# Performance work log

Hardware: AMD Instinct MI355X
Metric: run time of the kernel (lower is better)

The kernel has to match this reference:

```python
import jax, jax.numpy as jnp
import numpy as np


def _lstm_dir(xz, Uh, reverse):
    """Run one LSTM direction. xz: [B,T,4U] = x@W + b precomputed. Uh: [U,4U].
    activation='sigmoid' (replaces tanh on candidate and cell output),
    recurrent_activation='sigmoid' (Keras default). Gate order: i, f, g, o."""
    B = xz.shape[0]
    units = Uh.shape[0]
    h0 = jnp.zeros((B, units), xz.dtype)
    c0 = jnp.zeros((B, units), xz.dtype)

    def step(carry, z_t):
        h, c = carry
        z = z_t + h @ Uh                      # [B,4U]
        i, f, g, o = jnp.split(z, 4, axis=-1)
        i = jax.nn.sigmoid(i)
        f = jax.nn.sigmoid(f)
        g = jax.nn.sigmoid(g)                 # activation='sigmoid'
        o = jax.nn.sigmoid(o)
        c = f * c + i * g
        h = o * jax.nn.sigmoid(c)             # output activation also sigmoid
        return (h, c), h

    xz_t = jnp.swapaxes(xz, 0, 1)             # [T,B,4U]
    _, hs = jax.lax.scan(step, (h0, c0), xz_t, reverse=reverse)
    return jnp.swapaxes(hs, 0, 1)             # [B,T,U], time-ordered


def setup_inputs() -> dict:
    key = jax.random.key(0)
    k1, k2, k3 = jax.random.split(key, 3)
    B, T, D = 16, 1024, 1024
    L, U = 5, 512
    x = jax.random.normal(k1, (B, T, D), dtype=jnp.float32)
    # Glorot-ish scaling to keep sigmoids out of deep saturation
    W = jax.random.normal(k2, (L, 2, D, 4 * U), dtype=jnp.float32) * 0.03
    Uh = jax.random.normal(k3, (L, 2, U, 4 * U), dtype=jnp.float32) * 0.03
    b = jnp.zeros((L, 2, 4 * U), dtype=jnp.float32)
    return {"x": x, "W": W, "Uh": Uh, "b": b}


def reference(x, W, Uh, b):
    y = x
    n_layers = W.shape[0]
    for l in range(n_layers):
        outs = []
        for d, rev in ((0, False), (1, True)):
            # input projection for all timesteps at once (one big GEMM)
            xz = jnp.einsum('bti,io->bto', y, W[l, d]) + b[l, d]
            outs.append(_lstm_dir(xz, Uh[l, d], rev))
        y = jnp.concatenate(outs, axis=-1)    # Bidirectional merge_mode='concat'
    return y
```

## Files before the change

### kernel.cpp

```cpp
#include <hip/hip_runtime.h>
#include <hip/hip_bf16.h>
#include <stdint.h>


typedef __attribute__((ext_vector_type(8))) short short8;
typedef __attribute__((ext_vector_type(4))) float f32x4;

union U128 { uint4 u; short8 s; };
static __device__ __forceinline__ short8 as_short8(uint4 v) { U128 x; x.u = v; return x.s; }

static __device__ __forceinline__ float sigf(float x) { return 1.0f / (1.0f + __expf(-x)); }

static __device__ __forceinline__ uint32_t f2bfbits(float f) {
  union { float f; uint32_t u; } x; x.f = f;
  return (x.u + 0x7fffu + ((x.u >> 16) & 1u)) >> 16;
}
static __device__ __forceinline__ float bflo(uint32_t v) {
  union { uint32_t u; float f; } x; x.u = v << 16; return x.f;
}
static __device__ __forceinline__ float bfhi(uint32_t v) {
  union { uint32_t u; float f; } x; x.u = v & 0xffff0000u; return x.f;
}

__global__ __launch_bounds__(256) void f32_to_bf16_k(const float* __restrict__ in,
                                                     __hip_bfloat16* __restrict__ out,
                                                     int n4) {
  int i = blockIdx.x * 256 + threadIdx.x;
  if (i < n4) {
    float4 v = ((const float4*)in)[i];
    uint32_t lo = f2bfbits(v.x) | (f2bfbits(v.y) << 16);
    uint32_t hi = f2bfbits(v.z) | (f2bfbits(v.w) << 16);
    ((uint2*)out)[i] = make_uint2(lo, hi);
  }
}

__global__ __launch_bounds__(256) void transpose_bf16_k(const float* __restrict__ in,
                                                        __hip_bfloat16* __restrict__ outp,
                                                        int R) {
  __shared__ float tile[64][65];
  int d = blockIdx.z;
  int k0 = blockIdx.x * 64;
  int c0 = blockIdx.y * 64;
  const float* inb = in + (size_t)d * R * 2048;
  __hip_bfloat16* ob = outp + (size_t)d * 2048 * R;
  int col = threadIdx.x & 63, rr = threadIdx.x >> 6;
#pragma unroll
  for (int i = 0; i < 16; ++i) {
    int r = rr + i * 4;
    tile[r][col] = inb[(size_t)(k0 + r) * 2048 + c0 + col];
  }
  __syncthreads();
#pragma unroll
  for (int i = 0; i < 16; ++i) {
    int r = rr + i * 4;
    ob[(size_t)(c0 + r) * R + k0 + col] = __float2bfloat16(tile[col][r]);
  }
}

__global__ __launch_bounds__(256) void gemm_xz_k(const __hip_bfloat16* __restrict__ y,
                                                 const __hip_bfloat16* __restrict__ Wt,
                                                 const float* __restrict__ bias,
                                                 __hip_bfloat16* __restrict__ xz) {
  __shared__ uint4 Asl[8 * 2 * 64];
  __shared__ uint4 Bsl[8 * 2 * 64];
  int m0 = blockIdx.x * 128;
  int dir = blockIdx.y >> 4;
  int n0 = (blockIdx.y & 15) * 128;
  int tid = threadIdx.x, lane = tid & 63, wv = tid >> 6;
  int wm = wv & 1, wn = wv >> 1;
  const __hip_bfloat16* Wd = Wt + (size_t)dir * 2048 * 1024;
  f32x4 acc[4][4] = {};
  for (int kb = 0; kb < 1024; kb += 64) {
    __syncthreads();
#pragma unroll
    for (int i = 0; i < 4; ++i) {
      int slot = i * 256 + tid;
      int ln = slot & 63, kc = (slot >> 6) & 1, mt = slot >> 7;
      int row = mt * 16 + (ln & 15);
      int kk = kc * 32 + (ln >> 4) * 8;
      Asl[slot] = *(const uint4*)(y + (size_t)(m0 + row) * 1024 + kb + kk);
      Bsl[slot] = *(const uint4*)(Wd + (size_t)(n0 + row) * 1024 + kb + kk);
    }
    __syncthreads();
#pragma unroll
    for (int kc = 0; kc < 2; ++kc) {
      short8 af[4], bf[4];
#pragma unroll
      for (int i = 0; i < 4; ++i) {
        af[i] = as_short8(Asl[((wm * 4 + i) * 2 + kc) * 64 + lane]);
        bf[i] = as_short8(Bsl[((wn * 4 + i) * 2 + kc) * 64 + lane]);
      }
#pragma unroll
      for (int i = 0; i < 4; ++i)
#pragma unroll
        for (int j = 0; j < 4; ++j)
          acc[i][j] = __builtin_amdgcn_mfma_f32_16x16x32_bf16(af[i], bf[j], acc[i][j], 0, 0, 0);
    }
  }
  int cq = lane >> 4, cn = lane & 15;
#pragma unroll
  for (int i = 0; i < 4; ++i)
#pragma unroll
    for (int j = 0; j < 4; ++j) {
      int n_g = n0 + (wn * 4 + j) * 16 + cn;
      int q = n_g >> 9, u = n_g & 511, swg = u >> 5, jj = u & 31;
      float bv = bias[dir * 2048 + n_g];
#pragma unroll
      for (int r = 0; r < 4; ++r) {
        int m = m0 + (wm * 4 + i) * 16 + cq * 4 + r;
        int b = m >> 10, t = m & 1023;
        size_t addr = (((size_t)(dir * 16 + swg) * 1024 + t) * 2048) + (q * 16 + b) * 32 + jj;
        xz[addr] = __float2bfloat16(acc[i][j][r] + bv);
      }
    }
}

__global__ __launch_bounds__(256) void lstm_rec_k(const __hip_bfloat16* __restrict__ Ut,
                                                  const __hip_bfloat16* __restrict__ xz,
                                                  __hip_bfloat16* __restrict__ ynext,
                                                  float* __restrict__ outf) {
  extern __shared__ char smem[];
  uint4* uh = (uint4*)smem;
  __hip_bfloat16* hbuf = (__hip_bfloat16*)(smem + 131072);
  float* zbuf = (float*)(smem + 147712);
  __hip_bfloat16* xbuf = (__hip_bfloat16*)(smem + 156160);
  int dir = blockIdx.x & 1;
  int swg = blockIdx.x >> 1;
  int u0 = swg * 32;
  int tid = threadIdx.x, lane = tid & 63, wv = tid >> 6;
  int quad = lane >> 4, l15 = lane & 15;
  const __hip_bfloat16* Ud = Ut + (size_t)dir * 2048 * 512;

#pragma unroll 4
  for (int i = 0; i < 32; ++i) {
    int slot = i * 256 + tid;
    int ls = slot & 63, kc = (slot >> 6) & 15, nt = slot >> 10;
    int n_g = (nt >> 1) * 512 + u0 + (nt & 1) * 16 + (ls & 15);
    int k = kc * 32 + (ls >> 4) * 8;
    uh[slot] = *(const uint4*)(Ud + (size_t)n_g * 512 + k);
  }
  __syncthreads();

  int nt0 = wv * 2, nt1 = wv * 2 + 1;
  int pb = tid >> 4, pj = (tid & 15) * 2;
  float c0 = 0.f, c1 = 0.f;

  int t0 = dir ? 1023 : 0;
  const uint4* xp0 = (const uint4*)(xz + ((size_t)(dir * 16 + swg) * 1024 + t0) * 2048) + tid;
  uint4 xcur = *xp0;

  for (int s = 0; s < 1024; ++s) {
    int t = dir ? (1023 - s) : s;
    uint4 xnxt;
    if (s < 1023) {
      int tn = dir ? (1022 - s) : (s + 1);
      xnxt = *((const uint4*)(xz + ((size_t)(dir * 16 + swg) * 1024 + tn) * 2048) + tid);
    }
    f32x4 z0 = {}, z1 = {};
    if (s > 0) {
      int tprev = dir ? (t + 1) : (t - 1);
      unsigned long long hv[8];
      const unsigned long long* gp[8];
#pragma unroll
      for (int i = 0; i < 4; ++i) {
        int v = i * 2048 + tid * 8;
        int b = v >> 9, col = v & 511;
        const unsigned long long* g =
            (const unsigned long long*)(ynext + ((size_t)b * 1024 + tprev) * 1024 + dir * 512 + col);
        gp[2 * i] = g;
        gp[2 * i + 1] = g + 1;
      }
#pragma unroll
      for (int i = 0; i < 8; ++i)
        hv[i] = __hip_atomic_load(gp[i], __ATOMIC_RELAXED, __HIP_MEMORY_SCOPE_AGENT);
      for (;;) {
        bool ok = true;
#pragma unroll
        for (int i = 0; i < 8; ++i)
          ok &= ((uint32_t)hv[i] != 0u) && ((uint32_t)(hv[i] >> 32) != 0u);
        if (ok) break;
#pragma unroll
        for (int i = 0; i < 8; ++i)
          if (((uint32_t)hv[i] == 0u) || ((uint32_t)(hv[i] >> 32) == 0u))
            hv[i] = __hip_atomic_load(gp[i], __ATOMIC_RELAXED, __HIP_MEMORY_SCOPE_AGENT);
      }
#pragma unroll
      for (int i = 0; i < 4; ++i) {
        int v = i * 2048 + tid * 8;
        int b = v >> 9, col = v & 511;
        unsigned long long* lp = (unsigned long long*)(hbuf + b * 520 + col);
        lp[0] = hv[2 * i];
        lp[1] = hv[2 * i + 1];
      }
      __syncthreads();
#pragma unroll
      for (int kc = 0; kc < 16; ++kc) {
        short8 afrag = *(const short8*)(hbuf + l15 * 520 + kc * 32 + quad * 8);
        z0 = __builtin_amdgcn_mfma_f32_16x16x32_bf16(afrag, as_short8(uh[(nt0 * 16 + kc) * 64 + lane]), z0, 0, 0, 0);
        z1 = __builtin_amdgcn_mfma_f32_16x16x32_bf16(afrag, as_short8(uh[(nt1 * 16 + kc) * 64 + lane]), z1, 0, 0, 0);
      }
    }
#pragma unroll
    for (int r = 0; r < 4; ++r) {
      int m = quad * 4 + r;
      zbuf[m * 132 + nt0 * 16 + l15] = z0[r];
      zbuf[m * 132 + nt1 * 16 + l15] = z1[r];
    }
    *(uint4*)(xbuf + tid * 8) = xcur;
    __syncthreads();
    const float* zb = zbuf + pb * 132;
    uint32_t xi = *(const uint32_t*)(xbuf + (0 * 16 + pb) * 32 + pj);
    uint32_t xf = *(const uint32_t*)(xbuf + (1 * 16 + pb) * 32 + pj);
    uint32_t xg = *(const uint32_t*)(xbuf + (2 * 16 + pb) * 32 + pj);
    uint32_t xo = *(const uint32_t*)(xbuf + (3 * 16 + pb) * 32 + pj);
    float i0 = sigf(zb[pj] + bflo(xi)),      i1 = sigf(zb[pj + 1] + bfhi(xi));
    float f0 = sigf(zb[32 + pj] + bflo(xf)), f1 = sigf(zb[32 + pj + 1] + bfhi(xf));
    float g0 = sigf(zb[64 + pj] + bflo(xg)), g1 = sigf(zb[64 + pj + 1] + bfhi(xg));
    float o0 = sigf(zb[96 + pj] + bflo(xo)), o1 = sigf(zb[96 + pj + 1] + bfhi(xo));
    c0 = f0 * c0 + i0 * g0;
    c1 = f1 * c1 + i1 * g1;
    float h0 = o0 * sigf(c0);
    float h1 = o1 * sigf(c1);
    size_t oidx = ((size_t)pb * 1024 + t) * 1024 + dir * 512 + u0 + pj;
    uint32_t ha = f2bfbits(h0); ha += (ha == 0u);
    uint32_t hb = f2bfbits(h1); hb += (hb == 0u);
    uint32_t hp = ha | (hb << 16);
    __hip_atomic_store((uint32_t*)(ynext + oidx), hp, __ATOMIC_RELAXED, __HIP_MEMORY_SCOPE_AGENT);
    if (outf) { outf[oidx] = h0; outf[oidx + 1] = h1; }
    asm volatile("" ::: "memory");
    __builtin_amdgcn_s_barrier();
    xcur = xnxt;
  }
}

extern "C" void kernel_launch(void* const* d_in, const int* in_sizes, int n_in,
                              void* d_out, int out_size, void* d_ws, size_t ws_size,
                              hipStream_t stream) {
  const float* x  = (const float*)d_in[0];
  const float* W  = (const float*)d_in[1];
  const float* Uh = (const float*)d_in[2];
  const float* b  = (const float*)d_in[3];

  char* ws = (char*)d_ws;
  size_t off = 0;
  __hip_bfloat16* yA = (__hip_bfloat16*)(ws + off); off += (size_t)16 * 1024 * 1024 * 2;
  __hip_bfloat16* yB = (__hip_bfloat16*)(ws + off); off += (size_t)16 * 1024 * 1024 * 2;
  __hip_bfloat16* xz = (__hip_bfloat16*)(ws + off); off += (size_t)2 * 16 * 1024 * 2048 * 2;
  __hip_bfloat16* Wt = (__hip_bfloat16*)(ws + off); off += (size_t)2 * 2048 * 1024 * 2;
  __hip_bfloat16* Ut = (__hip_bfloat16*)(ws + off); off += (size_t)2 * 2048 * 512 * 2;

  f32_to_bf16_k<<<dim3(16384), dim3(256), 0, stream>>>(x, yA, 4194304);
  hipFuncSetAttribute(reinterpret_cast<const void*>(lstm_rec_k),
                      hipFuncAttributeMaxDynamicSharedMemorySize, 160256);
  for (int l = 0; l < 5; ++l) {
    transpose_bf16_k<<<dim3(16, 32, 2), dim3(256), 0, stream>>>(W + (size_t)l * 2 * 1024 * 2048, Wt, 1024);
    transpose_bf16_k<<<dim3(8, 32, 2),  dim3(256), 0, stream>>>(Uh + (size_t)l * 2 * 512 * 2048, Ut, 512);
    __hip_bfloat16* ycur = (l & 1) ? yB : yA;
    __hip_bfloat16* ynxt = (l & 1) ? yA : yB;
    hipMemsetAsync(ynxt, 0, (size_t)16 * 1024 * 1024 * 2, stream);
    gemm_xz_k<<<dim3(128, 32), dim3(256), 0, stream>>>(ycur, Wt, b + (size_t)l * 2 * 2048, xz);
    lstm_rec_k<<<dim3(32), dim3(256), 160256, stream>>>(
        Ut, xz, ynxt, (l == 4) ? (float*)d_out : nullptr);
  }
}
```

Baseline: 14.92 ms.

## Interleave forward and backward directions within each recurrent block

Each of the 32 recurrent blocks now owns a 16-unit slice of both directions instead of a 32-unit slice of one direction. It alternates a forward phase and a backward phase each step, so one direction's cross-block h exchange latency can hide behind the other's compute. The xz layout changes to 16-unit slices to match. Per phase, each wave does half the MFMAs and only half the threads do gate math, so there are more barriers and spin-waits per timestep in exchange for latency hiding.

```diff
diff --git a/kernel.cpp b/kernel.cpp
--- a/kernel.cpp
+++ b/kernel.cpp
@@ -103,16 +103,101 @@
 #pragma unroll
     for (int j = 0; j < 4; ++j) {
       int n_g = n0 + (wn * 4 + j) * 16 + cn;
-      int q = n_g >> 9, u = n_g & 511, swg = u >> 5, jj = u & 31;
+      int q = n_g >> 9, u = n_g & 511, sl = u >> 4, jj = u & 15;
       float bv = bias[dir * 2048 + n_g];
 #pragma unroll
       for (int r = 0; r < 4; ++r) {
         int m = m0 + (wm * 4 + i) * 16 + cq * 4 + r;
         int b = m >> 10, t = m & 1023;
-        size_t addr = (((size_t)(dir * 16 + swg) * 1024 + t) * 2048) + (q * 16 + b) * 32 + jj;
+        size_t addr = (((size_t)(dir * 32 + sl) * 1024 + t) * 1024) + (q * 16 + b) * 16 + jj;
         xz[addr] = __float2bfloat16(acc[i][j][r] + bv);
       }
     }
+}
+
+template <int D>
+static __device__ __forceinline__ void lstm_phase(
+    int s, int t, int slice, int tid, int lane, int wv, int quad, int l15,
+    const uint4* uh, __hip_bfloat16* hbuf, float* zbuf, __hip_bfloat16* xbuf,
+    const __hip_bfloat16* __restrict__ xz, __hip_bfloat16* __restrict__ ynext,
+    float* __restrict__ outf, uint2& xcur, float& c0, float& c1) {
+  uint2 xn = xcur;
+  if (s < 1023) {
+    int tn = D ? (t - 1) : (t + 1);
+    xn = *((const uint2*)(xz + ((size_t)(D * 32 + slice) * 1024 + tn) * 1024) + tid);
+  }
+  f32x4 z = {};
+  if (s > 0) {
+    int tprev = D ? (t + 1) : (t - 1);
+    unsigned long long hv[8];
+    const unsigned long long* gp[8];
+#pragma unroll
+    for (int i = 0; i < 4; ++i) {
+      int v = i * 2048 + tid * 8;
+      int b = v >> 9, col = v & 511;
+      const unsigned long long* g =
+          (const unsigned long long*)(ynext + ((size_t)b * 1024 + tprev) * 1024 + D * 512 + col);
+      gp[2 * i] = g; gp[2 * i + 1] = g + 1;
+    }
+#pragma unroll
+    for (int i = 0; i < 8; ++i)
+      hv[i] = __hip_atomic_load(gp[i], __ATOMIC_RELAXED, __HIP_MEMORY_SCOPE_AGENT);
+    for (;;) {
+      bool ok = true;
+#pragma unroll
+      for (int i = 0; i < 8; ++i)
+        ok &= ((uint32_t)hv[i] != 0u) && ((uint32_t)(hv[i] >> 32) != 0u);
+      if (ok) break;
+#pragma unroll
+      for (int i = 0; i < 8; ++i)
+        if (((uint32_t)hv[i] == 0u) || ((uint32_t)(hv[i] >> 32) == 0u))
+          hv[i] = __hip_atomic_load(gp[i], __ATOMIC_RELAXED, __HIP_MEMORY_SCOPE_AGENT);
+    }
+#pragma unroll
+    for (int i = 0; i < 4; ++i) {
+      int v = i * 2048 + tid * 8;
+      int b = v >> 9, col = v & 511;
+      unsigned long long* lp = (unsigned long long*)(hbuf + b * 520 + col);
+      lp[0] = hv[2 * i]; lp[1] = hv[2 * i + 1];
+    }
+    asm volatile("s_waitcnt lgkmcnt(0)\ns_barrier" ::: "memory");
+#pragma unroll
+    for (int kc = 0; kc < 16; ++kc) {
+      short8 afrag = *(const short8*)(hbuf + l15 * 520 + kc * 32 + quad * 8);
+      z = __builtin_amdgcn_mfma_f32_16x16x32_bf16(
+          afrag, as_short8(uh[((D * 4 + wv) * 16 + kc) * 64 + lane]), z, 0, 0, 0);
+    }
+  }
+#pragma unroll
+  for (int r = 0; r < 4; ++r)
+    zbuf[(quad * 4 + r) * 68 + wv * 16 + l15] = z[r];
+  *(uint2*)(xbuf + tid * 4) = xcur;
+  asm volatile("s_waitcnt lgkmcnt(0)\ns_barrier" ::: "memory");
+  if (tid < 128) {
+    int pb = tid >> 3, pj = (tid & 7) * 2;
+    const float* zb = zbuf + pb * 68;
+    uint32_t xi = *(const uint32_t*)(xbuf + (0 * 16 + pb) * 16 + pj);
+    uint32_t xf = *(const uint32_t*)(xbuf + (1 * 16 + pb) * 16 + pj);
+    uint32_t xg = *(const uint32_t*)(xbuf + (2 * 16 + pb) * 16 + pj);
+    uint32_t xo = *(const uint32_t*)(xbuf + (3 * 16 + pb) * 16 + pj);
+    float i0 = sigf(zb[pj] + bflo(xi)),      i1 = sigf(zb[pj + 1] + bfhi(xi));
+    float f0 = sigf(zb[16 + pj] + bflo(xf)), f1 = sigf(zb[16 + pj + 1] + bfhi(xf));
+    float g0 = sigf(zb[32 + pj] + bflo(xg)), g1 = sigf(zb[32 + pj + 1] + bfhi(xg));
+    float o0 = sigf(zb[48 + pj] + bflo(xo)), o1 = sigf(zb[48 + pj + 1] + bfhi(xo));
+    c0 = f0 * c0 + i0 * g0;
+    c1 = f1 * c1 + i1 * g1;
+    float h0 = o0 * sigf(c0);
+    float h1 = o1 * sigf(c1);
+    size_t oidx = ((size_t)pb * 1024 + t) * 1024 + D * 512 + slice * 16 + pj;
+    uint32_t ha = f2bfbits(h0); ha += (ha == 0u);
+    uint32_t hb = f2bfbits(h1); hb += (hb == 0u);
+    __hip_atomic_store((uint32_t*)(ynext + oidx), ha | (hb << 16),
+                       __ATOMIC_RELAXED, __HIP_MEMORY_SCOPE_AGENT);
+    if (outf) { outf[oidx] = h0; outf[oidx + 1] = h1; }
+  }
+  asm volatile("" ::: "memory");
+  if (s == 0) asm volatile("s_waitcnt lgkmcnt(0)\ns_barrier" ::: "memory");
+  xcur = xn;
 }
 
 __global__ __launch_bounds__(256) void lstm_rec_k(const __hip_bfloat16* __restrict__ Ut,
@@ -123,113 +208,31 @@
   uint4* uh = (uint4*)smem;
   __hip_bfloat16* hbuf = (__hip_bfloat16*)(smem + 131072);
   float* zbuf = (float*)(smem + 147712);
-  __hip_bfloat16* xbuf = (__hip_bfloat16*)(smem + 156160);
-  int dir = blockIdx.x & 1;
-  int swg = blockIdx.x >> 1;
-  int u0 = swg * 32;
+  __hip_bfloat16* xbuf = (__hip_bfloat16*)(smem + 152064);
+  int slice = blockIdx.x;
   int tid = threadIdx.x, lane = tid & 63, wv = tid >> 6;
   int quad = lane >> 4, l15 = lane & 15;
-  const __hip_bfloat16* Ud = Ut + (size_t)dir * 2048 * 512;
 
 #pragma unroll 4
   for (int i = 0; i < 32; ++i) {
     int slot = i * 256 + tid;
-    int ls = slot & 63, kc = (slot >> 6) & 15, nt = slot >> 10;
-    int n_g = (nt >> 1) * 512 + u0 + (nt & 1) * 16 + (ls & 15);
+    int ls = slot & 63, kc = (slot >> 6) & 15, w = (slot >> 10) & 3, d = slot >> 12;
+    int n_g = w * 512 + slice * 16 + (ls & 15);
     int k = kc * 32 + (ls >> 4) * 8;
-    uh[slot] = *(const uint4*)(Ud + (size_t)n_g * 512 + k);
+    uh[slot] = *(const uint4*)(Ut + ((size_t)d * 2048 + n_g) * 512 + k);
   }
   __syncthreads();
 
-  int nt0 = wv * 2, nt1 = wv * 2 + 1;
-  int pb = tid >> 4, pj = (tid & 15) * 2;
-  float c0 = 0.f, c1 = 0.f;
-
-  int t0 = dir ? 1023 : 0;
-  const uint4* xp0 = (const uint4*)(xz + ((size_t)(dir * 16 + swg) * 1024 + t0) * 2048) + tid;
-  uint4 xcur = *xp0;
+  float cf0 = 0.f, cf1 = 0.f, cb0 = 0.f, cb1 = 0.f;
+
+  uint2 xf = *((const uint2*)(xz + ((size_t)(0 * 32 + slice) * 1024 + 0) * 1024) + tid);
+  uint2 xb = *((const uint2*)(xz + ((size_t)(1 * 32 + slice) * 1024 + 1023) * 1024) + tid);
 
   for (int s = 0; s < 1024; ++s) {
-    int t = dir ? (1023 - s) : s;
-    uint4 xnxt;
-    if (s < 1023) {
-      int tn = dir ? (1022 - s) : (s + 1);
-      xnxt = *((const uint4*)(xz + ((size_t)(dir * 16 + swg) * 1024 + tn) * 2048) + tid);
-    }
-    f32x4 z0 = {}, z1 = {};
-    if (s > 0) {
-      int tprev = dir ? (t + 1) : (t - 1);
-      unsigned long long hv[8];
-      const unsigned long long* gp[8];
-#pragma unroll
-      for (int i = 0; i < 4; ++i) {
-        int v = i * 2048 + tid * 8;
-        int b = v >> 9, col = v & 511;
-        const unsigned long long* g =
-            (const unsigned long long*)(ynext + ((size_t)b * 1024 + tprev) * 1024 + dir * 512 + col);
-        gp[2 * i] = g;
-        gp[2 * i + 1] = g + 1;
-      }
-#pragma unroll
-      for (int i = 0; i < 8; ++i)
-        hv[i] = __hip_atomic_load(gp[i], __ATOMIC_RELAXED, __HIP_MEMORY_SCOPE_AGENT);
-      for (;;) {
-        bool ok = true;
-#pragma unroll
-        for (int i = 0; i < 8; ++i)
-          ok &= ((uint32_t)hv[i] != 0u) && ((uint32_t)(hv[i] >> 32) != 0u);
-        if (ok) break;
-#pragma unroll
-        for (int i = 0; i < 8; ++i)
-          if (((uint32_t)hv[i] == 0u) || ((uint32_t)(hv[i] >> 32) == 0u))
-            hv[i] = __hip_atomic_load(gp[i], __ATOMIC_RELAXED, __HIP_MEMORY_SCOPE_AGENT);
-      }
-#pragma unroll
-      for (int i = 0; i < 4; ++i) {
-        int v = i * 2048 + tid * 8;
-        int b = v >> 9, col = v & 511;
-        unsigned long long* lp = (unsigned long long*)(hbuf + b * 520 + col);
-        lp[0] = hv[2 * i];
-        lp[1] = hv[2 * i + 1];
-      }
-      __syncthreads();
-#pragma unroll
-      for (int kc = 0; kc < 16; ++kc) {
-        short8 afrag = *(const short8*)(hbuf + l15 * 520 + kc * 32 + quad * 8);
-        z0 = __builtin_amdgcn_mfma_f32_16x16x32_bf16(afrag, as_short8(uh[(nt0 * 16 + kc) * 64 + lane]), z0, 0, 0, 0);
-        z1 = __builtin_amdgcn_mfma_f32_16x16x32_bf16(afrag, as_short8(uh[(nt1 * 16 + kc) * 64 + lane]), z1, 0, 0, 0);
-      }
-    }
-#pragma unroll
-    for (int r = 0; r < 4; ++r) {
-      int m = quad * 4 + r;
-      zbuf[m * 132 + nt0 * 16 + l15] = z0[r];
-      zbuf[m * 132 + nt1 * 16 + l15] = z1[r];
-    }
-    *(uint4*)(xbuf + tid * 8) = xcur;
-    __syncthreads();
-    const float* zb = zbuf + pb * 132;
-    uint32_t xi = *(const uint32_t*)(xbuf + (0 * 16 + pb) * 32 + pj);
-    uint32_t xf = *(const uint32_t*)(xbuf + (1 * 16 + pb) * 32 + pj);
-    uint32_t xg = *(const uint32_t*)(xbuf + (2 * 16 + pb) * 32 + pj);
-    uint32_t xo = *(const uint32_t*)(xbuf + (3 * 16 + pb) * 32 + pj);
-    float i0 = sigf(zb[pj] + bflo(xi)),      i1 = sigf(zb[pj + 1] + bfhi(xi));
-    float f0 = sigf(zb[32 + pj] + bflo(xf)), f1 = sigf(zb[32 + pj + 1] + bfhi(xf));
-    float g0 = sigf(zb[64 + pj] + bflo(xg)), g1 = sigf(zb[64 + pj + 1] + bfhi(xg));
-    float o0 = sigf(zb[96 + pj] + bflo(xo)), o1 = sigf(zb[96 + pj + 1] + bfhi(xo));
-    c0 = f0 * c0 + i0 * g0;
-    c1 = f1 * c1 + i1 * g1;
-    float h0 = o0 * sigf(c0);
-    float h1 = o1 * sigf(c1);
-    size_t oidx = ((size_t)pb * 1024 + t) * 1024 + dir * 512 + u0 + pj;
-    uint32_t ha = f2bfbits(h0); ha += (ha == 0u);
-    uint32_t hb = f2bfbits(h1); hb += (hb == 0u);
-    uint32_t hp = ha | (hb << 16);
-    __hip_atomic_store((uint32_t*)(ynext + oidx), hp, __ATOMIC_RELAXED, __HIP_MEMORY_SCOPE_AGENT);
-    if (outf) { outf[oidx] = h0; outf[oidx + 1] = h1; }
-    asm volatile("" ::: "memory");
-    __builtin_amdgcn_s_barrier();
-    xcur = xnxt;
+    lstm_phase<0>(s, s,        slice, tid, lane, wv, quad, l15,
+                  uh, hbuf, zbuf, xbuf, xz, ynext, outf, xf, cf0, cf1);
+    lstm_phase<1>(s, 1023 - s, slice, tid, lane, wv, quad, l15,
+                  uh, hbuf, zbuf, xbuf, xz, ynext, outf, xb, cb0, cb1);
   }
 }
 
@@ -245,13 +248,13 @@
   size_t off = 0;
   __hip_bfloat16* yA = (__hip_bfloat16*)(ws + off); off += (size_t)16 * 1024 * 1024 * 2;
   __hip_bfloat16* yB = (__hip_bfloat16*)(ws + off); off += (size_t)16 * 1024 * 1024 * 2;
-  __hip_bfloat16* xz = (__hip_bfloat16*)(ws + off); off += (size_t)2 * 16 * 1024 * 2048 * 2;
+  __hip_bfloat16* xz = (__hip_bfloat16*)(ws + off); off += (size_t)2 * 32 * 1024 * 1024 * 2;
   __hip_bfloat16* Wt = (__hip_bfloat16*)(ws + off); off += (size_t)2 * 2048 * 1024 * 2;
   __hip_bfloat16* Ut = (__hip_bfloat16*)(ws + off); off += (size_t)2 * 2048 * 512 * 2;
 
   f32_to_bf16_k<<<dim3(16384), dim3(256), 0, stream>>>(x, yA, 4194304);
   hipFuncSetAttribute(reinterpret_cast<const void*>(lstm_rec_k),
-                      hipFuncAttributeMaxDynamicSharedMemorySize, 160256);
+                      hipFuncAttributeMaxDynamicSharedMemorySize, 154112);
   for (int l = 0; l < 5; ++l) {
     transpose_bf16_k<<<dim3(16, 32, 2), dim3(256), 0, stream>>>(W + (size_t)l * 2 * 1024 * 2048, Wt, 1024);
     transpose_bf16_k<<<dim3(8, 32, 2),  dim3(256), 0, stream>>>(Uh + (size_t)l * 2 * 512 * 2048, Ut, 512);
@@ -259,7 +262,7 @@
     __hip_bfloat16* ynxt = (l & 1) ? yA : yB;
     hipMemsetAsync(ynxt, 0, (size_t)16 * 1024 * 1024 * 2, stream);
     gemm_xz_k<<<dim3(128, 32), dim3(256), 0, stream>>>(ycur, Wt, b + (size_t)l * 2 * 2048, xz);
-    lstm_rec_k<<<dim3(32), dim3(256), 160256, stream>>>(
+    lstm_rec_k<<<dim3(32), dim3(256), 154112, stream>>>(
         Ut, xz, ynxt, (l == 4) ? (float*)d_out : nullptr);
   }
 }
```

Result: slower. 21.29 ms (+42.7%).
